# Kernel tuning notes

Measured on AMD Instinct MI355X. Metric: run time of the kernel, lower is better.

## Reference

```python
import jax, jax.numpy as jnp
import numpy as np

BLK = 64      # NF4 quantization blocksize
SUPER = 256   # double-quant blocksize over absmax

# NF4 codebook (bitsandbytes normal-float-4 lookup table)
NF4 = jnp.array([
    -1.0, -0.6961928009986877, -0.5250730514526367, -0.39491748809814453,
    -0.28444138169288635, -0.18477343022823334, -0.09105003625154495, 0.0,
    0.07958029955625534, 0.16093020141124725, 0.24611230194568634,
    0.33791524171829224, 0.44070982933044434, 0.5626170039176941,
    0.7229568362236023, 1.0], dtype=jnp.float32)


def setup_inputs() -> dict:
    key = jax.random.key(0)
    k1, k2, k3, k4, k5, k6 = jax.random.split(key, 6)
    B, S, I, O = 4, 2048, 4096, 4096
    n_blocks = O * I // BLK            # 262144
    n_super = n_blocks // SUPER        # 1024
    return {
        "x": jax.random.normal(k1, (B, S, I), dtype=jnp.float32),
        "w_codes": jax.random.randint(k2, (O, I), 0, 16, dtype=jnp.int32),
        "absmax_codes": jax.random.randint(k3, (n_blocks,), 0, 256, dtype=jnp.int32),
        "absmax_scale": jax.random.uniform(k4, (n_super,), dtype=jnp.float32),
        "absmax_offset": jax.random.uniform(k5, (1,), dtype=jnp.float32),
        "bias": jax.random.normal(k6, (O,), dtype=jnp.float32),
    }


def reference(x, w_codes, absmax_codes, absmax_scale, absmax_offset, bias):
    O, I = w_codes.shape
    # --- double-quant: dequantize 8-bit absmax codes blockwise (SUPER) ---
    # absmax[b] = code/255 * scale[superblock(b)] + offset
    am = absmax_codes.astype(jnp.float32) / 255.0          # [n_blocks]
    am = am.reshape(-1, SUPER) * absmax_scale[:, None] + absmax_offset[0]
    absmax = am.reshape(O, I // BLK)                        # per-64 block scale
    # --- NF4 dequant: lookup-table value * blockwise absmax ---
    w = NF4[w_codes].reshape(O, I // BLK, BLK) * absmax[:, :, None]
    w = w.reshape(O, I)                                     # [O, I] fp32
    # --- GEMM + bias (compute_dtype analog) ---
    return jnp.einsum('bsi,oi->bso', x, w) + bias
```

## Files before the change

### kernel.cpp

```cpp
#include <hip/hip_runtime.h>
#include <cstdint>
#include <cstddef>

#define DIM_M 8192
#define DIM_N 4096
#define DIM_K 4096

#define BM 256
#define BN 256
#define BK 32
#define NT (DIM_K / BK)

typedef __bf16 bf16x8 __attribute__((ext_vector_type(8)));
typedef float fvec4 __attribute__((ext_vector_type(4)));
typedef int   ivec4 __attribute__((ext_vector_type(4)));
typedef unsigned int uvec4 __attribute__((ext_vector_type(4)));

__device__ __constant__ float NF4_TAB[16] = {
    -1.0f, -0.6961928009986877f, -0.5250730514526367f, -0.39491748809814453f,
    -0.28444138169288635f, -0.18477343022823334f, -0.09105003625154495f, 0.0f,
    0.07958029955625534f, 0.16093020141124725f, 0.24611230194568634f,
    0.33791524171829224f, 0.44070982933044434f, 0.5626170039176941f,
    0.7229568362236023f, 1.0f};

__device__ inline unsigned short f2bf(float f) {
    unsigned int u = __builtin_bit_cast(unsigned int, f);
    u += 0x7fffu + ((u >> 16) & 1u);
    return (unsigned short)(u >> 16);
}

__global__ void prep_kernel(const float* __restrict__ x, unsigned short* __restrict__ xb,
                            const int* __restrict__ codes,
                            const int* __restrict__ am_codes,
                            const float* __restrict__ am_scale,
                            const float* __restrict__ am_off,
                            unsigned short* __restrict__ wb,
                            int xcv_blocks) {
    if ((int)blockIdx.x < xcv_blocks) {
        size_t base = ((size_t)blockIdx.x * blockDim.x + threadIdx.x) * 8;
        fvec4 a = __builtin_nontemporal_load((const fvec4*)(x + base));
        fvec4 b = __builtin_nontemporal_load((const fvec4*)(x + base + 4));
        unsigned short r[8];
        r[0] = f2bf(a.x); r[1] = f2bf(a.y); r[2] = f2bf(a.z); r[3] = f2bf(a.w);
        r[4] = f2bf(b.x); r[5] = f2bf(b.y); r[6] = f2bf(b.z); r[7] = f2bf(b.w);
        *(uvec4*)(xb + base) = *(const uvec4*)r;
    } else {
        __shared__ float nf4[16];
        if (threadIdx.x < 16) nf4[threadIdx.x] = NF4_TAB[threadIdx.x];
        __syncthreads();
        size_t base = ((size_t)(blockIdx.x - xcv_blocks) * blockDim.x + threadIdx.x) * 8;
        int blk = (int)(base >> 6);
        float absmax = (float)am_codes[blk] * (1.0f / 255.0f) * am_scale[blk >> 8] + am_off[0];
        ivec4 c0 = __builtin_nontemporal_load((const ivec4*)(codes + base));
        ivec4 c1 = __builtin_nontemporal_load((const ivec4*)(codes + base + 4));
        unsigned short r[8];
        r[0] = f2bf(nf4[c0.x & 15] * absmax);
        r[1] = f2bf(nf4[c0.y & 15] * absmax);
        r[2] = f2bf(nf4[c0.z & 15] * absmax);
        r[3] = f2bf(nf4[c0.w & 15] * absmax);
        r[4] = f2bf(nf4[c1.x & 15] * absmax);
        r[5] = f2bf(nf4[c1.y & 15] * absmax);
        r[6] = f2bf(nf4[c1.z & 15] * absmax);
        r[7] = f2bf(nf4[c1.w & 15] * absmax);
        *(uvec4*)(wb + base) = *(const uvec4*)r;
    }
}

__device__ inline void gld_lds16(const void* g, void* l) {
    __builtin_amdgcn_global_load_lds((__attribute__((address_space(1))) void*)g,
                                     (__attribute__((address_space(3))) void*)l,
                                     16, 0, 0);
}

__global__ __launch_bounds__(512, 2) void gemm_bt(const unsigned short* __restrict__ A,
                                                  const unsigned short* __restrict__ B,
                                                  const float* __restrict__ bias,
                                                  float* __restrict__ C,
                                                  int M, int N, int K) {
    __shared__ __attribute__((aligned(16))) unsigned short lA[4][BM * BK];
    __shared__ __attribute__((aligned(16))) unsigned short lB[4][BN * BK];

    const int tid  = threadIdx.x;
    const int wave = tid >> 6;
    const int lane = tid & 63;

    const int orig = (int)blockIdx.x;
    const int xcd = orig & 7;
    const int idx = orig >> 3;
    const int bm = ((idx >> 4) << 3) + xcd;
    const int bn = idx & 15;

    const int wr = wave >> 2;
    const int wc = wave & 3;
    const int wm = wr * 128;
    const int wn = wc * 64;

    const int srow = tid >> 2;
    const int gch  = (tid & 3) ^ ((tid >> 3) & 3);
    const unsigned short* sA0 = A + (size_t)(bm * BM + srow) * K + gch * 8;
    const unsigned short* sA1 = sA0 + (size_t)128 * K;
    const unsigned short* sB0 = B + (size_t)(bn * BN + srow) * K + gch * 8;
    const unsigned short* sB1 = sB0 + (size_t)128 * K;

    const int cslot = (lane >> 4) ^ ((lane >> 1) & 3);
    const int aoff = (wm + (lane & 15)) * BK + cslot * 8;
    const int boff = (wn + (lane & 15)) * BK + cslot * 8;

    fvec4 acc[8][4];
#pragma unroll
    for (int m = 0; m < 8; ++m)
#pragma unroll
        for (int n = 0; n < 4; ++n)
#pragma unroll
            for (int r = 0; r < 4; ++r) acc[m][n][r] = 0.0f;

#pragma unroll
    for (int pt = 0; pt < 3; ++pt) {
        const int kb = pt * BK;
        gld_lds16(sA0 + kb, &lA[pt][tid * 8]);
        gld_lds16(sA1 + kb, &lA[pt][(tid + 512) * 8]);
        gld_lds16(sB0 + kb, &lB[pt][tid * 8]);
        gld_lds16(sB1 + kb, &lB[pt][(tid + 512) * 8]);
    }
    asm volatile("s_waitcnt vmcnt(8)" ::: "memory");
    __builtin_amdgcn_s_barrier();

    for (int t = 0; t < NT; ++t) {
        const int b = t & 3;
        const unsigned short* la = lA[b];
        const unsigned short* lb = lB[b];

        bf16x8 a0[4], bv[4];
#pragma unroll
        for (int m = 0; m < 4; ++m) a0[m] = *(const bf16x8*)(la + aoff + m * 512);
#pragma unroll
        for (int n = 0; n < 4; ++n) bv[n] = *(const bf16x8*)(lb + boff + n * 512);
        if (t + 3 < NT) {
            const int nb = (t + 3) & 3;
            const size_t kb = (size_t)(t + 3) * BK;
            gld_lds16(sA0 + kb, &lA[nb][tid * 8]);
            gld_lds16(sA1 + kb, &lA[nb][(tid + 512) * 8]);
        }
        __builtin_amdgcn_s_barrier();
        asm volatile("s_waitcnt lgkmcnt(0)" ::: "memory");
        __builtin_amdgcn_sched_barrier(0);
        __builtin_amdgcn_s_setprio(1);
#pragma unroll
        for (int m = 0; m < 4; ++m)
#pragma unroll
            for (int n = 0; n < 4; ++n)
                acc[m][n] = __builtin_amdgcn_mfma_f32_16x16x32_bf16(a0[m], bv[n], acc[m][n], 0, 0, 0);
        __builtin_amdgcn_s_setprio(0);
        __builtin_amdgcn_s_barrier();

        bf16x8 a1[4];
#pragma unroll
        for (int m = 0; m < 4; ++m) a1[m] = *(const bf16x8*)(la + aoff + (m + 4) * 512);
        if (t + 3 < NT) {
            const int nb = (t + 3) & 3;
            const size_t kb = (size_t)(t + 3) * BK;
            gld_lds16(sB0 + kb, &lB[nb][tid * 8]);
            gld_lds16(sB1 + kb, &lB[nb][(tid + 512) * 8]);
        }
        __builtin_amdgcn_s_barrier();
        asm volatile("s_waitcnt lgkmcnt(0)" ::: "memory");
        __builtin_amdgcn_sched_barrier(0);
        __builtin_amdgcn_s_setprio(1);
#pragma unroll
        for (int m = 0; m < 4; ++m)
#pragma unroll
            for (int n = 0; n < 4; ++n)
                acc[m + 4][n] = __builtin_amdgcn_mfma_f32_16x16x32_bf16(a1[m], bv[n], acc[m + 4][n], 0, 0, 0);
        __builtin_amdgcn_s_setprio(0);

        if (t < NT - 3)       { asm volatile("s_waitcnt vmcnt(8)" ::: "memory"); }
        else if (t == NT - 3) { asm volatile("s_waitcnt vmcnt(4)" ::: "memory"); }
        else if (t == NT - 2) { asm volatile("s_waitcnt vmcnt(0)" ::: "memory"); }
        if (t < NT - 1) __builtin_amdgcn_s_barrier();
    }

    const int col0 = bn * BN + wn + (lane & 15);
    const int row0 = bm * BM + wm + ((lane >> 4) << 2);
#pragma unroll
    for (int n = 0; n < 4; ++n) {
        const float bvs = bias[col0 + n * 16];
#pragma unroll
        for (int m = 0; m < 8; ++m) {
            float* cp = C + (size_t)(row0 + m * 16) * N + col0 + n * 16;
#pragma unroll
            for (int r = 0; r < 4; ++r)
                __builtin_nontemporal_store(acc[m][n][r] + bvs, cp + (size_t)r * N);
        }
    }
}

extern "C" void kernel_launch(void* const* d_in, const int* in_sizes, int n_in,
                              void* d_out, int out_size, void* d_ws, size_t ws_size,
                              hipStream_t stream) {
    const float* x        = (const float*)d_in[0];
    const int*   w_codes  = (const int*)d_in[1];
    const int*   am_codes = (const int*)d_in[2];
    const float* am_scale = (const float*)d_in[3];
    const float* am_off   = (const float*)d_in[4];
    const float* bias     = (const float*)d_in[5];
    float* out = (float*)d_out;

    const int M = DIM_M, N = DIM_N, K = DIM_K;

    unsigned short* xb = (unsigned short*)d_ws;
    unsigned short* wb = xb + (size_t)M * K;

    {
        int xcv_blocks = (int)(((size_t)M * K) / 8 / 256);
        int wdq_blocks = (int)(((size_t)N * K) / 8 / 256);
        prep_kernel<<<xcv_blocks + wdq_blocks, 256, 0, stream>>>(
            x, xb, w_codes, am_codes, am_scale, am_off, wb, xcv_blocks);
    }
    {
        dim3 grid((M / BM) * (N / BN));
        gemm_bt<<<grid, 512, 0, stream>>>(xb, wb, bias, out, M, N, K);
    }
}
```

Measured before the change: 509.5 us.

## Restructure GEMM main loop to one barrier per tile with 4x unroll

Result: faster. 484.8 us (-4.8%).

```diff
diff --git a/kernel.cpp b/kernel.cpp
--- a/kernel.cpp
+++ b/kernel.cpp
@@ -90,10 +90,8 @@
     const int bm = ((idx >> 4) << 3) + xcd;
     const int bn = idx & 15;
 
-    const int wr = wave >> 2;
-    const int wc = wave & 3;
-    const int wm = wr * 128;
-    const int wn = wc * 64;
+    const int wm = (wave >> 2) * 128;
+    const int wn = (wave & 3) * 64;
 
     const int srow = tid >> 2;
     const int gch  = (tid & 3) ^ ((tid >> 3) & 3);
@@ -125,55 +123,76 @@
     asm volatile("s_waitcnt vmcnt(8)" ::: "memory");
     __builtin_amdgcn_s_barrier();
 
-    for (int t = 0; t < NT; ++t) {
+#define TILE_MAIN(J)                                                                   \
+    do {                                                                               \
+        constexpr int BUF = (J) & 3;                                                   \
+        constexpr int NBUF = (BUF + 3) & 3;                                            \
+        gld_lds16(pA0 + (J) * BK, &lA[NBUF][tid * 8]);                                 \
+        gld_lds16(pA1 + (J) * BK, &lA[NBUF][(tid + 512) * 8]);                         \
+        gld_lds16(pB0 + (J) * BK, &lB[NBUF][tid * 8]);                                 \
+        gld_lds16(pB1 + (J) * BK, &lB[NBUF][(tid + 512) * 8]);                         \
+        bf16x8 a0[4], a1[4], bv[4];                                                    \
+        _Pragma("unroll") for (int m = 0; m < 4; ++m)                                  \
+            a0[m] = *(const bf16x8*)(&lA[BUF][0] + aoff + m * 512);                    \
+        _Pragma("unroll") for (int n = 0; n < 4; ++n)                                  \
+            bv[n] = *(const bf16x8*)(&lB[BUF][0] + boff + n * 512);                    \
+        _Pragma("unroll") for (int m = 0; m < 4; ++m)                                  \
+            a1[m] = *(const bf16x8*)(&lA[BUF][0] + aoff + (m + 4) * 512);              \
+        __builtin_amdgcn_s_setprio(1);                                                 \
+        _Pragma("unroll") for (int m = 0; m < 4; ++m)                                  \
+            _Pragma("unroll") for (int n = 0; n < 4; ++n)                              \
+                acc[m][n] = __builtin_amdgcn_mfma_f32_16x16x32_bf16(a0[m], bv[n], acc[m][n], 0, 0, 0); \
+        _Pragma("unroll") for (int m = 0; m < 4; ++m)                                  \
+            _Pragma("unroll") for (int n = 0; n < 4; ++n)                              \
+                acc[m + 4][n] = __builtin_amdgcn_mfma_f32_16x16x32_bf16(a1[m], bv[n], acc[m + 4][n], 0, 0, 0); \
+        __builtin_amdgcn_s_setprio(0);                                                 \
+        asm volatile("s_waitcnt vmcnt(8)" ::: "memory");                               \
+        __builtin_amdgcn_s_barrier();                                                  \
+    } while (0)
+
+    {
+        const unsigned short* pA0 = sA0 + 3 * BK;
+        const unsigned short* pA1 = sA1 + 3 * BK;
+        const unsigned short* pB0 = sB0 + 3 * BK;
+        const unsigned short* pB1 = sB1 + 3 * BK;
+        for (int t0 = 0; t0 < NT - 4; t0 += 4) {
+            TILE_MAIN(0);
+            TILE_MAIN(1);
+            TILE_MAIN(2);
+            TILE_MAIN(3);
+            pA0 += 4 * BK; pA1 += 4 * BK; pB0 += 4 * BK; pB1 += 4 * BK;
+        }
+    }
+
+    for (int t = NT - 4; t < NT; ++t) {
         const int b = t & 3;
-        const unsigned short* la = lA[b];
-        const unsigned short* lb = lB[b];
-
-        bf16x8 a0[4], bv[4];
-#pragma unroll
-        for (int m = 0; m < 4; ++m) a0[m] = *(const bf16x8*)(la + aoff + m * 512);
-#pragma unroll
-        for (int n = 0; n < 4; ++n) bv[n] = *(const bf16x8*)(lb + boff + n * 512);
         if (t + 3 < NT) {
-            const int nb = (t + 3) & 3;
             const size_t kb = (size_t)(t + 3) * BK;
-            gld_lds16(sA0 + kb, &lA[nb][tid * 8]);
-            gld_lds16(sA1 + kb, &lA[nb][(tid + 512) * 8]);
+            gld_lds16(sA0 + kb, &lA[(b + 3) & 3][tid * 8]);
+            gld_lds16(sA1 + kb, &lA[(b + 3) & 3][(tid + 512) * 8]);
+            gld_lds16(sB0 + kb, &lB[(b + 3) & 3][tid * 8]);
+            gld_lds16(sB1 + kb, &lB[(b + 3) & 3][(tid + 512) * 8]);
         }
-        __builtin_amdgcn_s_barrier();
-        asm volatile("s_waitcnt lgkmcnt(0)" ::: "memory");
-        __builtin_amdgcn_sched_barrier(0);
+        bf16x8 a0[4], a1[4], bv[4];
+#pragma unroll
+        for (int m = 0; m < 4; ++m) a0[m] = *(const bf16x8*)(&lA[b][0] + aoff + m * 512);
+#pragma unroll
+        for (int n = 0; n < 4; ++n) bv[n] = *(const bf16x8*)(&lB[b][0] + boff + n * 512);
+#pragma unroll
+        for (int m = 0; m < 4; ++m) a1[m] = *(const bf16x8*)(&lA[b][0] + aoff + (m + 4) * 512);
         __builtin_amdgcn_s_setprio(1);
 #pragma unroll
         for (int m = 0; m < 4; ++m)
 #pragma unroll
             for (int n = 0; n < 4; ++n)
                 acc[m][n] = __builtin_amdgcn_mfma_f32_16x16x32_bf16(a0[m], bv[n], acc[m][n], 0, 0, 0);
-        __builtin_amdgcn_s_setprio(0);
-        __builtin_amdgcn_s_barrier();
-
-        bf16x8 a1[4];
-#pragma unroll
-        for (int m = 0; m < 4; ++m) a1[m] = *(const bf16x8*)(la + aoff + (m + 4) * 512);
-        if (t + 3 < NT) {
-            const int nb = (t + 3) & 3;
-            const size_t kb = (size_t)(t + 3) * BK;
-            gld_lds16(sB0 + kb, &lB[nb][tid * 8]);
-            gld_lds16(sB1 + kb, &lB[nb][(tid + 512) * 8]);
-        }
-        __builtin_amdgcn_s_barrier();
-        asm volatile("s_waitcnt lgkmcnt(0)" ::: "memory");
-        __builtin_amdgcn_sched_barrier(0);
-        __builtin_amdgcn_s_setprio(1);
 #pragma unroll
         for (int m = 0; m < 4; ++m)
 #pragma unroll
             for (int n = 0; n < 4; ++n)
                 acc[m + 4][n] = __builtin_amdgcn_mfma_f32_16x16x32_bf16(a1[m], bv[n], acc[m + 4][n], 0, 0, 0);
         __builtin_amdgcn_s_setprio(0);
-
-        if (t < NT - 3)       { asm volatile("s_waitcnt vmcnt(8)" ::: "memory"); }
+        if (t == NT - 4)      { asm volatile("s_waitcnt vmcnt(8)" ::: "memory"); }
         else if (t == NT - 3) { asm volatile("s_waitcnt vmcnt(4)" ::: "memory"); }
         else if (t == NT - 2) { asm volatile("s_waitcnt vmcnt(0)" ::: "memory"); }
         if (t < NT - 1) __builtin_amdgcn_s_barrier();
```

## Double-buffer LDS fragments in registers and unroll GEMM main loop by four

Applied to the files above, without the earlier changes.

New measurement: 528.5 us. 1.04x slower.

```diff
diff --git a/kernel.cpp b/kernel.cpp
--- a/kernel.cpp
+++ b/kernel.cpp
@@ -38,8 +38,8 @@
                             int xcv_blocks) {
     if ((int)blockIdx.x < xcv_blocks) {
         size_t base = ((size_t)blockIdx.x * blockDim.x + threadIdx.x) * 8;
-        fvec4 a = __builtin_nontemporal_load((const fvec4*)(x + base));
-        fvec4 b = __builtin_nontemporal_load((const fvec4*)(x + base + 4));
+        fvec4 a = *(const fvec4*)(x + base);
+        fvec4 b = *(const fvec4*)(x + base + 4);
         unsigned short r[8];
         r[0] = f2bf(a.x); r[1] = f2bf(a.y); r[2] = f2bf(a.z); r[3] = f2bf(a.w);
         r[4] = f2bf(b.x); r[5] = f2bf(b.y); r[6] = f2bf(b.z); r[7] = f2bf(b.w);
@@ -51,8 +51,8 @@
         size_t base = ((size_t)(blockIdx.x - xcv_blocks) * blockDim.x + threadIdx.x) * 8;
         int blk = (int)(base >> 6);
         float absmax = (float)am_codes[blk] * (1.0f / 255.0f) * am_scale[blk >> 8] + am_off[0];
-        ivec4 c0 = __builtin_nontemporal_load((const ivec4*)(codes + base));
-        ivec4 c1 = __builtin_nontemporal_load((const ivec4*)(codes + base + 4));
+        ivec4 c0 = *(const ivec4*)(codes + base);
+        ivec4 c1 = *(const ivec4*)(codes + base + 4);
         unsigned short r[8];
         r[0] = f2bf(nf4[c0.x & 15] * absmax);
         r[1] = f2bf(nf4[c0.y & 15] * absmax);
@@ -90,10 +90,8 @@
     const int bm = ((idx >> 4) << 3) + xcd;
     const int bn = idx & 15;
 
-    const int wr = wave >> 2;
-    const int wc = wave & 3;
-    const int wm = wr * 128;
-    const int wn = wc * 64;
+    const int wm = (wave >> 2) * 128;
+    const int wn = (wave & 3) * 64;
 
     const int srow = tid >> 2;
     const int gch  = (tid & 3) ^ ((tid >> 3) & 3);
@@ -114,6 +112,8 @@
 #pragma unroll
             for (int r = 0; r < 4; ++r) acc[m][n][r] = 0.0f;
 
+    bf16x8 fa0[8], fb0[4], fa1[8], fb1[4];
+
 #pragma unroll
     for (int pt = 0; pt < 3; ++pt) {
         const int kb = pt * BK;
@@ -122,61 +122,116 @@
         gld_lds16(sB0 + kb, &lB[pt][tid * 8]);
         gld_lds16(sB1 + kb, &lB[pt][(tid + 512) * 8]);
     }
-    asm volatile("s_waitcnt vmcnt(8)" ::: "memory");
+    asm volatile("s_waitcnt vmcnt(4)" ::: "memory");
     __builtin_amdgcn_s_barrier();
-
-    for (int t = 0; t < NT; ++t) {
-        const int b = t & 3;
-        const unsigned short* la = lA[b];
-        const unsigned short* lb = lB[b];
-
-        bf16x8 a0[4], bv[4];
-#pragma unroll
-        for (int m = 0; m < 4; ++m) a0[m] = *(const bf16x8*)(la + aoff + m * 512);
-#pragma unroll
-        for (int n = 0; n < 4; ++n) bv[n] = *(const bf16x8*)(lb + boff + n * 512);
-        if (t + 3 < NT) {
-            const int nb = (t + 3) & 3;
-            const size_t kb = (size_t)(t + 3) * BK;
-            gld_lds16(sA0 + kb, &lA[nb][tid * 8]);
-            gld_lds16(sA1 + kb, &lA[nb][(tid + 512) * 8]);
+#pragma unroll
+    for (int m = 0; m < 8; ++m) fa0[m] = *(const bf16x8*)(&lA[0][0] + aoff + m * 512);
+#pragma unroll
+    for (int n = 0; n < 4; ++n) fb0[n] = *(const bf16x8*)(&lB[0][0] + boff + n * 512);
+
+#define REGION(J, FAc, FBc, FAn, FBn)                                                  \
+    do {                                                                               \
+        constexpr int SBUF = ((J) + 3) & 3;                                            \
+        constexpr int RBUF = ((J) + 1) & 3;                                            \
+        gld_lds16(pA0 + (J) * BK, &lA[SBUF][tid * 8]);                                 \
+        gld_lds16(pA1 + (J) * BK, &lA[SBUF][(tid + 512) * 8]);                         \
+        gld_lds16(pB0 + (J) * BK, &lB[SBUF][tid * 8]);                                 \
+        gld_lds16(pB1 + (J) * BK, &lB[SBUF][(tid + 512) * 8]);                         \
+        _Pragma("unroll") for (int m = 0; m < 8; ++m)                                  \
+            FAn[m] = *(const bf16x8*)(&lA[RBUF][0] + aoff + m * 512);                  \
+        _Pragma("unroll") for (int n = 0; n < 4; ++n)                                  \
+            FBn[n] = *(const bf16x8*)(&lB[RBUF][0] + boff + n * 512);                  \
+        asm volatile("s_waitcnt lgkmcnt(12)" ::: "memory");                            \
+        __builtin_amdgcn_sched_barrier(0);                                             \
+        __builtin_amdgcn_s_setprio(1);                                                 \
+        _Pragma("unroll") for (int m = 0; m < 8; ++m)                                  \
+            _Pragma("unroll") for (int n = 0; n < 4; ++n)                              \
+                acc[m][n] = __builtin_amdgcn_mfma_f32_16x16x32_bf16(FAc[m], FBc[n], acc[m][n], 0, 0, 0); \
+        __builtin_amdgcn_s_setprio(0);                                                 \
+        asm volatile("s_waitcnt vmcnt(4)" ::: "memory");                               \
+        __builtin_amdgcn_s_barrier();                                                  \
+    } while (0)
+
+    {
+        const unsigned short* pA0 = sA0 + 3 * BK;
+        const unsigned short* pA1 = sA1 + 3 * BK;
+        const unsigned short* pB0 = sB0 + 3 * BK;
+        const unsigned short* pB1 = sB1 + 3 * BK;
+        for (int t0 = 0; t0 < NT - 4; t0 += 4) {
+            REGION(0, fa0, fb0, fa1, fb1);
+            REGION(1, fa1, fb1, fa0, fb0);
+            REGION(2, fa0, fb0, fa1, fb1);
+            REGION(3, fa1, fb1, fa0, fb0);
+            pA0 += 4 * BK; pA1 += 4 * BK; pB0 += 4 * BK; pB1 += 4 * BK;
         }
+    }
+
+    {
+        const unsigned short* pA0 = sA0 + 127 * BK;
+        const unsigned short* pA1 = sA1 + 127 * BK;
+        const unsigned short* pB0 = sB0 + 127 * BK;
+        const unsigned short* pB1 = sB1 + 127 * BK;
+
+        gld_lds16(pA0, &lA[3][tid * 8]);
+        gld_lds16(pA1, &lA[3][(tid + 512) * 8]);
+        gld_lds16(pB0, &lB[3][tid * 8]);
+        gld_lds16(pB1, &lB[3][(tid + 512) * 8]);
+#pragma unroll
+        for (int m = 0; m < 8; ++m) fa1[m] = *(const bf16x8*)(&lA[1][0] + aoff + m * 512);
+#pragma unroll
+        for (int n = 0; n < 4; ++n) fb1[n] = *(const bf16x8*)(&lB[1][0] + boff + n * 512);
+        asm volatile("s_waitcnt lgkmcnt(12)" ::: "memory");
+        __builtin_amdgcn_sched_barrier(0);
+        __builtin_amdgcn_s_setprio(1);
+#pragma unroll
+        for (int m = 0; m < 8; ++m)
+#pragma unroll
+            for (int n = 0; n < 4; ++n)
+                acc[m][n] = __builtin_amdgcn_mfma_f32_16x16x32_bf16(fa0[m], fb0[n], acc[m][n], 0, 0, 0);
+        __builtin_amdgcn_s_setprio(0);
+        asm volatile("s_waitcnt vmcnt(4)" ::: "memory");
         __builtin_amdgcn_s_barrier();
+
+#pragma unroll
+        for (int m = 0; m < 8; ++m) fa0[m] = *(const bf16x8*)(&lA[2][0] + aoff + m * 512);
+#pragma unroll
+        for (int n = 0; n < 4; ++n) fb0[n] = *(const bf16x8*)(&lB[2][0] + boff + n * 512);
+        asm volatile("s_waitcnt lgkmcnt(12)" ::: "memory");
+        __builtin_amdgcn_sched_barrier(0);
+        __builtin_amdgcn_s_setprio(1);
+#pragma unroll
+        for (int m = 0; m < 8; ++m)
+#pragma unroll
+            for (int n = 0; n < 4; ++n)
+                acc[m][n] = __builtin_amdgcn_mfma_f32_16x16x32_bf16(fa1[m], fb1[n], acc[m][n], 0, 0, 0);
+        __builtin_amdgcn_s_setprio(0);
+        asm volatile("s_waitcnt vmcnt(0)" ::: "memory");
+        __builtin_amdgcn_s_barrier();
+
+#pragma unroll
+        for (int m = 0; m < 8; ++m) fa1[m] = *(const bf16x8*)(&lA[3][0] + aoff + m * 512);
+#pragma unroll
+        for (int n = 0; n < 4; ++n) fb1[n] = *(const bf16x8*)(&lB[3][0] + boff + n * 512);
+        asm volatile("s_waitcnt lgkmcnt(12)" ::: "memory");
+        __builtin_amdgcn_sched_barrier(0);
+        __builtin_amdgcn_s_setprio(1);
+#pragma unroll
+        for (int m = 0; m < 8; ++m)
+#pragma unroll
+            for (int n = 0; n < 4; ++n)
+                acc[m][n] = __builtin_amdgcn_mfma_f32_16x16x32_bf16(fa0[m], fb0[n], acc[m][n], 0, 0, 0);
+        __builtin_amdgcn_s_setprio(0);
+        __builtin_amdgcn_s_barrier();
+
         asm volatile("s_waitcnt lgkmcnt(0)" ::: "memory");
         __builtin_amdgcn_sched_barrier(0);
         __builtin_amdgcn_s_setprio(1);
 #pragma unroll
-        for (int m = 0; m < 4; ++m)
-#pragma unroll
-            for (int n = 0; n < 4; ++n)
-                acc[m][n] = __builtin_amdgcn_mfma_f32_16x16x32_bf16(a0[m], bv[n], acc[m][n], 0, 0, 0);
-        __builtin_amdgcn_s_setprio(0);
-        __builtin_amdgcn_s_barrier();
-
-        bf16x8 a1[4];
-#pragma unroll
-        for (int m = 0; m < 4; ++m) a1[m] = *(const bf16x8*)(la + aoff + (m + 4) * 512);
-        if (t + 3 < NT) {
-            const int nb = (t + 3) & 3;
-            const size_t kb = (size_t)(t + 3) * BK;
-            gld_lds16(sB0 + kb, &lB[nb][tid * 8]);
-            gld_lds16(sB1 + kb, &lB[nb][(tid + 512) * 8]);
-        }
-        __builtin_amdgcn_s_barrier();
-        asm volatile("s_waitcnt lgkmcnt(0)" ::: "memory");
-        __builtin_amdgcn_sched_barrier(0);
-        __builtin_amdgcn_s_setprio(1);
-#pragma unroll
-        for (int m = 0; m < 4; ++m)
-#pragma unroll
-            for (int n = 0; n < 4; ++n)
-                acc[m + 4][n] = __builtin_amdgcn_mfma_f32_16x16x32_bf16(a1[m], bv[n], acc[m + 4][n], 0, 0, 0);
-        __builtin_amdgcn_s_setprio(0);
-
-        if (t < NT - 3)       { asm volatile("s_waitcnt vmcnt(8)" ::: "memory"); }
-        else if (t == NT - 3) { asm volatile("s_waitcnt vmcnt(4)" ::: "memory"); }
-        else if (t == NT - 2) { asm volatile("s_waitcnt vmcnt(0)" ::: "memory"); }
-        if (t < NT - 1) __builtin_amdgcn_s_barrier();
+        for (int m = 0; m < 8; ++m)
+#pragma unroll
+            for (int n = 0; n < 4; ++n)
+                acc[m][n] = __builtin_amdgcn_mfma_f32_16x16x32_bf16(fa1[m], fb1[n], acc[m][n], 0, 0, 0);
+        __builtin_amdgcn_s_setprio(0);
     }
 
     const int col0 = bn * BN + wn + (lane & 15);
```
